# Optimization experiments

Hardware: AMD Instinct MI355X
Metric: run time of the kernel (lower is better)

## Reference

```python
import jax, jax.numpy as jnp
import numpy as np

C = 320        # in_channels == inner_dim (n_heads*d_head = 8*40)
HEADS = 8
DH = 40
CTX = 768
FF_INNER = 1280  # 4*C
G = 32         # GroupNorm groups


def _ln(x, w, b, eps=1e-5):
    m = x.mean(-1, keepdims=True)
    v = ((x - m) ** 2).mean(-1, keepdims=True)
    return (x - m) * jax.lax.rsqrt(v + eps) * w + b


def _attn(q, k, v, heads, scale):
    # faithful to source: split last dim as (d h) -> head index is fastest
    B, Lq, D = q.shape
    Lk = k.shape[1]
    dh = D // heads
    q = q.reshape(B, Lq, dh, heads).transpose(0, 3, 1, 2)  # b h i d
    k = k.reshape(B, Lk, dh, heads).transpose(0, 3, 1, 2)  # b h j d
    v = v.reshape(B, Lk, dh, heads).transpose(0, 3, 1, 2)
    sim = jnp.einsum('bhid,bhjd->bhij', q, k) * scale
    w = jax.nn.softmax(sim, axis=-1)
    o = jnp.einsum('bhij,bhjd->bhid', w, v)
    # merge as (h d): head index is slowest on output (matches source)
    return o.transpose(0, 2, 1, 3).reshape(B, Lq, heads * dh)


def setup_inputs() -> dict:
    key = jax.random.key(0)
    ks = jax.random.split(key, 20)
    n = lambda i, shape: jax.random.normal(ks[i], shape, jnp.float32) * 0.02
    z = lambda d: jnp.zeros((d,), jnp.float32)
    o = lambda d: jnp.ones((d,), jnp.float32)
    return dict(
        x=jax.random.normal(ks[0], (1, C, 64, 64), jnp.float32),
        context=jax.random.normal(ks[1], (1, 77, CTX), jnp.float32),
        gn_w=o(C), gn_b=z(C),
        w_in=n(2, (C, C)), b_in=z(C),
        ln1_w=o(C), ln1_b=z(C),
        wq1=n(3, (C, C)), wk1=n(4, (C, C)), wv1=n(5, (C, C)),
        wo1=n(6, (C, C)), bo1=z(C),
        ln2_w=o(C), ln2_b=z(C),
        wq2=n(7, (C, C)), wk2=n(8, (CTX, C)), wv2=n(9, (CTX, C)),
        wo2=n(10, (C, C)), bo2=z(C),
        ln3_w=o(C), ln3_b=z(C),
        wff1=n(11, (C, 2 * FF_INNER)), bff1=z(2 * FF_INNER),
        wff2=n(12, (FF_INNER, C)), bff2=z(C),
        w_out=n(13, (C, C)), b_out=z(C),
    )


def reference(x, context, gn_w, gn_b, w_in, b_in,
              ln1_w, ln1_b, wq1, wk1, wv1, wo1, bo1,
              ln2_w, ln2_b, wq2, wk2, wv2, wo2, bo2,
              ln3_w, ln3_b, wff1, bff1, wff2, bff2,
              w_out, b_out):
    B, Cc, H, W = x.shape
    scale = DH ** (-0.5)
    x_in = x
    # GroupNorm(32, eps=1e-6)
    g = x.reshape(B, G, Cc // G, H, W)
    m = g.mean((2, 3, 4), keepdims=True)
    v = ((g - m) ** 2).mean((2, 3, 4), keepdims=True)
    h = ((g - m) * jax.lax.rsqrt(v + 1e-6)).reshape(B, Cc, H, W)
    h = h * gn_w[None, :, None, None] + gn_b[None, :, None, None]
    # 1x1 conv in_proj
    h = jnp.einsum('bchw,co->bohw', h, w_in) + b_in[None, :, None, None]
    # b c h w -> b (h w) c
    t = h.transpose(0, 2, 3, 1).reshape(B, H * W, C)
    # --- transformer block (depth=1) ---
    # attn_1: self-attn; NOTE source applies k/v proj to the QUERY projection
    hn = _ln(t, ln1_w, ln1_b)
    q = hn @ wq1
    k = q @ wk1
    vv = q @ wv1
    t = t + (_attn(q, k, vv, HEADS, scale) @ wo1 + bo1)
    # attn_2: cross-attn with context
    hn = _ln(t, ln2_w, ln2_b)
    q = hn @ wq2
    k = context @ wk2
    vv = context @ wv2
    t = t + (_attn(q, k, vv, HEADS, scale) @ wo2 + bo2)
    # GEGLU feed-forward
    hn = _ln(t, ln3_w, ln3_b)
    p = hn @ wff1 + bff1
    a, gate = p[..., :FF_INNER], p[..., FF_INNER:]
    t = t + ((a * jax.nn.gelu(gate, approximate=False)) @ wff2 + bff2)
    # b (h w) c -> b c h w
    s = t.reshape(B, H, W, C).transpose(0, 3, 1, 2)
    out = jnp.einsum('bchw,co->bohw', s, w_out) + b_out[None, :, None, None]
    return out + x_in
```

## Files before the change

### kernel.cpp

```cpp
#include <hip/hip_runtime.h>
#include <hip/hip_bf16.h>
#include <math.h>

#define CCH 320
#define NHEADS 8
#define DH 40
#define HW 4096
#define FFI 1280

typedef __bf16 bf16x8 __attribute__((ext_vector_type(8)));
typedef unsigned short u16x8 __attribute__((ext_vector_type(8)));
typedef short s16x4 __attribute__((ext_vector_type(4)));
typedef float f32x4 __attribute__((ext_vector_type(4)));
typedef unsigned int u32x4 __attribute__((ext_vector_type(4)));

#define WQ1BF_OFF 2539520
#define W2_OFF    2641920
#define WT_TOTAL  2949120

__device__ inline unsigned short f2bf(float f) {
    __hip_bfloat16 h = __float2bfloat16(f);
    return __builtin_bit_cast(unsigned short, h);
}
__device__ inline unsigned pk2bf(float a, float b) {
#if __has_builtin(__builtin_amdgcn_cvt_pk_bf16_f32)
    typedef __bf16 bf16x2 __attribute__((ext_vector_type(2)));
    bf16x2 r = __builtin_amdgcn_cvt_pk_bf16_f32(a, b);
    return __builtin_bit_cast(unsigned, r);
#else
    return (unsigned)f2bf(a) | ((unsigned)f2bf(b) << 16);
#endif
}
__device__ inline float bf2f(unsigned short u) {
    return __builtin_bit_cast(float, ((unsigned)u) << 16);
}
__device__ inline bf16x8 ldfrag(const unsigned short* p) {
    u16x8 raw = *reinterpret_cast<const u16x8*>(p);
    return __builtin_bit_cast(bf16x8, raw);
}
__device__ inline s16x4 pk2frag(unsigned a, unsigned b) {
    unsigned long long v = (unsigned long long)a | ((unsigned long long)b << 32);
    return __builtin_bit_cast(s16x4, v);
}

__device__ inline float ex2(float x) {
#if __has_builtin(__builtin_amdgcn_exp2f)
    return __builtin_amdgcn_exp2f(x);
#else
    return exp2f(x);
#endif
}
__device__ inline float fast_rcp(float x) {
#if __has_builtin(__builtin_amdgcn_rcpf)
    return __builtin_amdgcn_rcpf(x);
#else
    return 1.f / x;
#endif
}
__device__ inline float fast_gelu(float x) {
    float z = fabsf(x) * 0.70710678118654752f;
    float t = fast_rcp(fmaf(0.3275911f, z, 1.f));
    float poly = fmaf(fmaf(fmaf(fmaf(1.061405429f, t, -1.453152027f), t,
                               1.421413741f), t, -0.284496736f), t,
                      0.254829592f) * t;
    float e = ex2(z * z * -1.4426950408889634f);
    float erfz = 1.f - poly * e;
    float s = copysignf(erfz, x);
    return 0.5f * x * (1.f + s);
}

__global__ __launch_bounds__(256) void megaprep(
    const float* __restrict__ w_in, const float* __restrict__ wq1,
    const float* __restrict__ wk1, const float* __restrict__ wv1,
    const float* __restrict__ wo1, const float* __restrict__ wq2,
    const float* __restrict__ wo2, const float* __restrict__ w_out,
    const float* __restrict__ wff1, const float* __restrict__ wff2,
    const float* __restrict__ wk2, const float* __restrict__ wv2,
    unsigned short* __restrict__ Wt,
    const float* __restrict__ ctx, unsigned short* __restrict__ ctx_bf,
    const float* __restrict__ X, float2* __restrict__ gnp) {
    __shared__ float tile[64][65];
    __shared__ float s1[256], s2[256];
    const int b = blockIdx.x, tid = threadIdx.x;
    if (b >= 670) {
        if (b < 1054) {
            int idx = (b - 670) * 256 + tid;
            int row = idx / 768, col = idx - row * 768;
            float v = (row < 77) ? ctx[row * 768 + col] : 0.f;
            ctx_bf[idx] = f2bf(v);
        } else {
            const int bg = b - 1054;
            const float* xg = X + bg * 5120;
            float s = 0.f, sq = 0.f;
#pragma unroll
            for (int i = 0; i < 20; ++i) { float v = xg[tid + i * 256]; s += v; sq += v * v; }
            s1[tid] = s; s2[tid] = sq; __syncthreads();
            for (int off = 128; off > 0; off >>= 1) {
                if (tid < off) { s1[tid] += s1[tid + off]; s2[tid] += s2[tid + off]; }
                __syncthreads();
            }
            if (tid == 0) gnp[bg] = make_float2(s1[0], s2[0]);
        }
        return;
    }
    if (b >= 620 && b < 645) {
        int t = b - 620;
        int base = (t / 5) * 64 * 320 + (t % 5) * 64;
#pragma unroll
        for (int i = 0; i < 16; ++i) {
            int idx = tid + i * 256;
            int r = idx >> 6, cn = idx & 63;
            Wt[WQ1BF_OFF + base + r * 320 + cn] = f2bf(wq1[base + r * 320 + cn]);
        }
        return;
    }
    const float* src;
    int K, stride, dstoff, k0, n0;
    bool glu = false;
    if (b < 200) {
        int m = b / 25, t = b % 25;
        k0 = (t / 5) * 64; n0 = (t % 5) * 64;
        K = 320; stride = 320; dstoff = m * 102400;
        src = (m == 0) ? w_in : (m == 1) ? wq1 : (m == 2) ? wk1 :
              (m == 3) ? wv1 : (m == 4) ? wo1 : (m == 5) ? wq2 :
              (m == 6) ? wo2 : w_out;
    } else if (b < 300) {
        int t = b - 200;
        k0 = (t / 5) * 64; n0 = (t % 5) * 64;
        K = 1280; stride = 320; dstoff = 1638400; src = wff2;
    } else if (b < 500) {
        int t = b - 300;
        k0 = (t / 40) * 64; n0 = (t % 40) * 64;
        K = 320; stride = 2560; dstoff = 819200; src = wff1; glu = true;
    } else if (b < 560) {
        int t = b - 500;
        k0 = (t / 5) * 64; n0 = (t % 5) * 64;
        K = 768; stride = 320; dstoff = 2048000; src = wk2;
    } else if (b < 620) {
        int t = b - 560;
        k0 = (t / 5) * 64; n0 = (t % 5) * 64;
        K = 768; stride = 320; dstoff = 2048000 + 245760; src = wv2;
    } else {
        int t = b - 645;
        k0 = (t / 5) * 64; n0 = (t % 5) * 64;
        K = 320; stride = 320; dstoff = W2_OFF; src = wq1;
    }
#pragma unroll
    for (int i = 0; i < 16; ++i) {
        int idx = tid + i * 256;
        int r = idx >> 6, cn = idx & 63;
        int scol = glu ? ((n0 >> 1) + (cn >> 1) + (cn & 1) * FFI) : (n0 + cn);
        tile[r][cn] = src[(size_t)(k0 + r) * stride + scol];
    }
    __syncthreads();
#pragma unroll
    for (int i = 0; i < 16; ++i) {
        int idx = tid + i * 256;
        int cl = idx >> 6, cr = idx & 63;
        Wt[dstoff + (size_t)(n0 + cl) * K + k0 + cr] = f2bf(tile[cr][cl]);
    }
}

__global__ __launch_bounds__(256) void gn_apply(const float* __restrict__ X,
                                                const float2* __restrict__ part,
                                                const float* __restrict__ w,
                                                const float* __restrict__ b,
                                                unsigned short* __restrict__ Y) {
    __shared__ float tile[64][65];
    __shared__ float gm[32], gr[32];
    const int tid = threadIdx.x;
    const int hw0 = blockIdx.x * 64, c0 = blockIdx.y * 64;
    if (tid < 32) {
        float s = 0.f, sq = 0.f;
#pragma unroll
        for (int i = 0; i < 8; ++i) { float2 p = part[tid * 8 + i]; s += p.x; sq += p.y; }
        float mean = s * (1.f / 40960.f);
        float var  = sq * (1.f / 40960.f) - mean * mean;
        gm[tid] = mean; gr[tid] = rsqrtf(var + 1e-6f);
    }
#pragma unroll
    for (int i = 0; i < 16; ++i) {
        int idx = tid + i * 256;
        int r = idx >> 6, col = idx & 63;
        tile[r][col] = X[(size_t)(c0 + r) * HW + hw0 + col];
    }
    __syncthreads();
#pragma unroll
    for (int i = 0; i < 16; ++i) {
        int idx = tid + i * 256;
        int hwl = idx >> 6, cl = idx & 63;
        int c = c0 + cl, g = c / 10;
        float v = (tile[cl][hwl] - gm[g]) * gr[g] * w[c] + b[c];
        Y[(size_t)(hw0 + hwl) * CCH + c] = f2bf(v);
    }
}

__global__ __launch_bounds__(256) void ln_kernel(const float* __restrict__ X,
                                                 const float* __restrict__ w,
                                                 const float* __restrict__ b,
                                                 unsigned short* __restrict__ Y) {
    const int row  = blockIdx.x * 4 + (threadIdx.x >> 6);
    const int lane = threadIdx.x & 63;
    const float* xr = X + row * CCH;
    const float4 a = *(const float4*)(xr + lane * 4);
    const float  e = xr[256 + lane];
    float v[5] = {a.x, a.y, a.z, a.w, e};
    float s = 0.f, sq = 0.f;
#pragma unroll
    for (int i = 0; i < 5; ++i) { s += v[i]; sq += v[i] * v[i]; }
#pragma unroll
    for (int off = 32; off > 0; off >>= 1) {
        s  += __shfl_xor(s, off, 64);
        sq += __shfl_xor(sq, off, 64);
    }
    const float mean = s * (1.f / 320.f);
    const float var  = sq * (1.f / 320.f) - mean * mean;
    const float rstd = rsqrtf(var + 1e-5f);
    unsigned short* yr = Y + row * CCH;
    const float4 w4 = *(const float4*)(w + lane * 4);
    const float4 b4 = *(const float4*)(b + lane * 4);
    float r0 = (v[0] - mean) * rstd * w4.x + b4.x;
    float r1 = (v[1] - mean) * rstd * w4.y + b4.y;
    float r2 = (v[2] - mean) * rstd * w4.z + b4.z;
    float r3 = (v[3] - mean) * rstd * w4.w + b4.w;
    *(uint2*)(yr + lane * 4) = make_uint2(pk2bf(r0, r1), pk2bf(r2, r3));
    int ct = 256 + lane;
    yr[ct] = f2bf((v[4] - mean) * rstd * w[ct] + b[ct]);
}

template <int MT, int K>
__global__ __launch_bounds__(256) void gemm4(
    const unsigned short* __restrict__ A,
    const unsigned short* __restrict__ Bt,
    const float* __restrict__ bias,
    const float* __restrict__ res,
    void* __restrict__ Cout, void* __restrict__ Cout2,
    int N, int mode, float scale) {
    constexpr int NCH = K / 64;
    __shared__ __align__(16) unsigned short Ab[2][MT * 16 * 64];
    __shared__ __align__(16) unsigned short Bb[2][64 * 64];
    const int tid  = threadIdx.x;
    const int wave = tid >> 6, lane = tid & 63;
    const int quad = lane >> 4, c = lane & 15;
    const int m0 = blockIdx.y * (MT * 16);
    const int bn = blockIdx.x;

    f32x4 acc[MT];
#pragma unroll
    for (int i = 0; i < MT; ++i) acc[i] = (f32x4){0.f, 0.f, 0.f, 0.f};

    const unsigned short* aslab = A + (size_t)m0 * K;
    const unsigned short* bslab = Bt + (size_t)(bn * 64) * K;

    constexpr int ITA = MT * 16 * 8 / 256;
    int arow[ITA], aoff[ITA];
#pragma unroll
    for (int i = 0; i < ITA; ++i) {
        int idx = tid + i * 256;
        arow[i] = idx >> 3;
        int g = idx & 7;
        aoff[i] = arow[i] * 64 + ((g ^ (arow[i] & 7)) * 8);
    }
    int brow[2], boff[2];
#pragma unroll
    for (int i = 0; i < 2; ++i) {
        int idx = tid + i * 256;
        brow[i] = idx >> 3;
        int g = idx & 7;
        boff[i] = brow[i] * 64 + ((g ^ (brow[i] & 7)) * 8);
    }
    const int ag = (tid & 7) * 8;

    {
        u16x8 ra[ITA], rb[2];
#pragma unroll
        for (int i = 0; i < ITA; ++i)
            ra[i] = *(const u16x8*)(aslab + (size_t)arow[i] * K + ag);
#pragma unroll
        for (int i = 0; i < 2; ++i)
            rb[i] = *(const u16x8*)(bslab + (size_t)brow[i] * K + ag);
#pragma unroll
        for (int i = 0; i < ITA; ++i) *(u16x8*)&Ab[0][aoff[i]] = ra[i];
#pragma unroll
        for (int i = 0; i < 2; ++i) *(u16x8*)&Bb[0][boff[i]] = rb[i];
    }
    __syncthreads();

    const int swz0 = (quad ^ (c & 7)) * 8;
    const int swz1 = ((quad + 4) ^ (c & 7)) * 8;
#pragma unroll
    for (int ch = 0; ch < NCH; ++ch) {
        const int buf = ch & 1;
        u16x8 ra[ITA], rb[2];
        if (ch + 1 < NCH) {
            const int kb = (ch + 1) * 64;
#pragma unroll
            for (int i = 0; i < ITA; ++i)
                ra[i] = *(const u16x8*)(aslab + (size_t)arow[i] * K + kb + ag);
#pragma unroll
            for (int i = 0; i < 2; ++i)
                rb[i] = *(const u16x8*)(bslab + (size_t)brow[i] * K + kb + ag);
        }
        bf16x8 b0 = ldfrag(&Bb[buf][(wave * 16 + c) * 64 + swz0]);
        bf16x8 b1 = ldfrag(&Bb[buf][(wave * 16 + c) * 64 + swz1]);
#pragma unroll
        for (int mt = 0; mt < MT; ++mt) {
            bf16x8 a0 = ldfrag(&Ab[buf][(mt * 16 + c) * 64 + swz0]);
            bf16x8 a1 = ldfrag(&Ab[buf][(mt * 16 + c) * 64 + swz1]);
            acc[mt] = __builtin_amdgcn_mfma_f32_16x16x32_bf16(a0, b0, acc[mt], 0, 0, 0);
            acc[mt] = __builtin_amdgcn_mfma_f32_16x16x32_bf16(a1, b1, acc[mt], 0, 0, 0);
        }
        if (ch + 1 < NCH) {
            const int nb = buf ^ 1;
#pragma unroll
            for (int i = 0; i < ITA; ++i) *(u16x8*)&Ab[nb][aoff[i]] = ra[i];
#pragma unroll
            for (int i = 0; i < 2; ++i) *(u16x8*)&Bb[nb][boff[i]] = rb[i];
        }
        __syncthreads();
    }

    const int col = bn * 64 + wave * 16 + c;
    float bval = 0.f;
    if (bias) bval = (mode == 5) ? bias[(col >> 1) + (col & 1) * FFI] : bias[col];

    if (mode == 9) {
#pragma unroll
        for (int mt = 0; mt < MT; ++mt) {
            const int row0 = m0 + mt * 16 + quad * 4;
            float4 xv = *(const float4*)(res + (size_t)col * HW + row0);
            float4 ov;
            ov.x = acc[mt][0] + bval + xv.x;
            ov.y = acc[mt][1] + bval + xv.y;
            ov.z = acc[mt][2] + bval + xv.z;
            ov.w = acc[mt][3] + bval + xv.w;
            *(float4*)((float*)Cout + (size_t)col * HW + row0) = ov;
        }
        return;
    }
#pragma unroll
    for (int mt = 0; mt < MT; ++mt) {
#pragma unroll
        for (int r = 0; r < 4; ++r) {
            const int row = m0 + mt * 16 + quad * 4 + r;
            float v = acc[mt][r];
            if (mode == 0) {
                v += bval;
                if (res) v += res[(size_t)row * N + col];
                ((float*)Cout)[(size_t)row * N + col] = v;
            } else if (mode == 2) {
                int h = col & 7, d = col >> 3;
                ((unsigned short*)Cout)[(((size_t)h << 12) + row) * 64 + d] = f2bf(v * scale);
                if (d < 24)
                    ((unsigned short*)Cout)[(((size_t)h << 12) + row) * 64 + 40 + d] = 0;
            } else if (mode == 4) {
                ((unsigned short*)Cout)[(size_t)row * N + col] =
                    f2bf(v + bval + res[(size_t)row * N + col]);
            } else if (mode == 5) {
                v += bval;
                float other = __shfl_xor(v, 1, 64);
                if ((c & 1) == 0) {
                    float g = fast_gelu(other);
                    ((unsigned short*)Cout)[(size_t)row * FFI + (col >> 1)] = f2bf(v * g);
                }
            } else if (mode == 8) {
                if (col < 320) {
                    int h = col & 7, d = col >> 3;
                    ((unsigned short*)Cout)[(((size_t)h << 7) + row) * 64 + d] = f2bf(v);
                    if (d < 24)
                        ((unsigned short*)Cout)[(((size_t)h << 7) + row) * 64 + 40 + d] = 0;
                } else {
                    int c2 = col - 320;
                    int h = c2 & 7, d = c2 >> 3;
                    ((unsigned short*)Cout2)[(size_t)(h * 48 + d) * 128 + row] = f2bf(v);
                    if (d < 8)
                        ((unsigned short*)Cout2)[(size_t)(h * 48 + 40 + d) * 128 + row] =
                            (d == 0) ? (unsigned short)0x3F80 : (unsigned short)0;
                }
            } else if (mode == 10) {
                ((unsigned short*)Cout)[(size_t)col * 320 + row] = f2bf(v);
            } else {
                if (col < 320) {
                    int h = col & 7, d = col >> 3;
                    ((unsigned short*)Cout)[(((size_t)h << 12) + row) * 64 + d] = f2bf(v * scale);
                    if (d < 24)
                        ((unsigned short*)Cout)[(((size_t)h << 12) + row) * 64 + 40 + d] = 0;
                } else if (col < 640) {
                    int c2 = col - 320;
                    int h = c2 & 7, d = c2 >> 3;
                    ((unsigned short*)Cout2)[(((size_t)h << 12) + row) * 64 + d] = f2bf(v);
                    if (d < 24)
                        ((unsigned short*)Cout2)[(((size_t)h << 12) + row) * 64 + 40 + d] = 0;
                } else {
                    int c2 = col - 640;
                    int h = c2 & 7, d = c2 >> 3;
                    unsigned short* Vt_ = (unsigned short*)Cout2 + (size_t)8 * 4096 * 64;
                    Vt_[(((size_t)(h * 48 + d)) << 12) + row] = f2bf(v);
                    if (d < 8)
                        Vt_[(((size_t)(h * 48 + 40 + d)) << 12) + row] =
                            (d == 0) ? (unsigned short)0x3F80 : (unsigned short)0;
                }
            }
        }
    }
}

template <int TILES, bool MASK, bool FINAL>
__global__ __launch_bounds__(256) void attn8(
    const unsigned short* __restrict__ Qp,
    const unsigned short* __restrict__ Kp,
    const unsigned short* __restrict__ Vt,
    float* __restrict__ pO, float* __restrict__ pL,
    unsigned short* __restrict__ Ofin,
    int Lk, int Lkp) {
    __shared__ __align__(16) unsigned short Kb[2][64 * 64];
    __shared__ __align__(16) unsigned short Vb[2][48 * 64];
    const int tid  = threadIdx.x;
    const int wave = tid >> 6, lane = tid & 63;
    const int quad = lane >> 4, c = lane & 15;
    const int id  = blockIdx.x;
    const int h   = id & 7;
    const int qt  = (id >> 3) & 31;
    const int seg = id >> 8;
    const int q0  = qt * 128 + wave * 32;

    const unsigned short* qbaseA = Qp + ((((size_t)h << 12) + q0 + c) << 6) + quad * 8;
    const bf16x8 bQA0 = ldfrag(qbaseA);
    const bf16x8 bQA1 = ldfrag(qbaseA + 32);
    const bf16x8 bQB0 = ldfrag(qbaseA + 1024);
    const bf16x8 bQB1 = ldfrag(qbaseA + 1024 + 32);

    f32x4 oA[3], oB[3];
#pragma unroll
    for (int i = 0; i < 3; ++i) {
        oA[i] = (f32x4){0.f, 0.f, 0.f, 0.f};
        oB[i] = (f32x4){0.f, 0.f, 0.f, 0.f};
    }

    const int kt0 = seg * TILES;
    const unsigned short* kglob = Kp + (((size_t)h * Lkp + kt0 * 64) << 6);
    const unsigned short* vglob = Vt + ((size_t)h * 48) * Lkp + kt0 * 64;

    const int r0 = lane >> 3;
    const int g  = lane & 7;
    int ldsoff[4];
    const unsigned short* gptr0[4];
#pragma unroll
    for (int i = 0; i < 4; ++i) {
        int s = wave + 4 * i;
        if (s < 8) {
            int row = s * 8 + r0;
            ldsoff[i] = row * 64 + (g ^ (row & 7)) * 8;
            gptr0[i]  = kglob + (size_t)row * 64 + g * 8;
        } else if (s < 14) {
            int d = (s - 8) * 8 + r0;
            ldsoff[i] = d * 64 + (g ^ (d & 7)) * 8;
            gptr0[i]  = vglob + (size_t)d * Lkp + g * 8;
        } else {
            ldsoff[i] = 0; gptr0[i] = nullptr;
        }
    }
    const bool isK[4] = {(wave + 0) < 8, (wave + 4) < 8, (wave + 8) < 8, (wave + 12) < 8};
    const bool act[4] = {true, true, true, (wave + 12) < 14};

    {
        u16x8 st[4];
#pragma unroll
        for (int i = 0; i < 4; ++i)
            if (act[i]) st[i] = *(const u16x8*)(gptr0[i]);
#pragma unroll
        for (int i = 0; i < 4; ++i)
            if (act[i]) {
                unsigned short* lp = isK[i] ? &Kb[0][ldsoff[i]] : &Vb[0][ldsoff[i]];
                *(u16x8*)lp = st[i];
            }
    }
    __syncthreads();

#pragma unroll
    for (int t = 0; t < TILES; ++t) {
        const int b = t & 1;
        u16x8 st[4];
        if (t + 1 < TILES) {
            const int kb = (t + 1) * 64;
#pragma unroll
            for (int i = 0; i < 4; ++i)
                if (act[i]) {
                    const unsigned short* gp =
                        isK[i] ? (gptr0[i] + (size_t)kb * 64) : (gptr0[i] + kb);
                    st[i] = *(const u16x8*)gp;
                }
        }
        const unsigned short* Kl = &Kb[b][0];
        const unsigned short* Vl = &Vb[b][0];
        const int sw0 = (quad ^ (c & 7)) * 8;
        const int sw1 = ((quad + 4) ^ (c & 7)) * 8;
        const int abs_kb = kt0 * 64 + t * 64;
#pragma unroll
        for (int blk = 0; blk < 4; ++blk) {
            const int row = (blk * 16 + c) * 64;
            bf16x8 k0 = ldfrag(Kl + row + sw0);
            bf16x8 k1 = ldfrag(Kl + row + sw1);
            f32x4 zA = {0.f, 0.f, 0.f, 0.f};
            zA = __builtin_amdgcn_mfma_f32_16x16x32_bf16(k0, bQA0, zA, 0, 0, 0);
            zA = __builtin_amdgcn_mfma_f32_16x16x32_bf16(k1, bQA1, zA, 0, 0, 0);
            f32x4 zB = {0.f, 0.f, 0.f, 0.f};
            zB = __builtin_amdgcn_mfma_f32_16x16x32_bf16(k0, bQB0, zB, 0, 0, 0);
            zB = __builtin_amdgcn_mfma_f32_16x16x32_bf16(k1, bQB1, zB, 0, 0, 0);
            if (MASK) {
#pragma unroll
                for (int r = 0; r < 4; ++r) {
                    bool inv = (abs_kb + blk * 16 + quad * 4 + r >= Lk);
                    zA[r] = inv ? -30000.f : zA[r];
                    zB[r] = inv ? -30000.f : zB[r];
                }
            }
            s16x4 PA = pk2frag(pk2bf(ex2(zA[0]), ex2(zA[1])),
                               pk2bf(ex2(zA[2]), ex2(zA[3])));
            s16x4 PB = pk2frag(pk2bf(ex2(zB[0]), ex2(zB[1])),
                               pk2bf(ex2(zB[2]), ex2(zB[3])));
#pragma unroll
            for (int db = 0; db < 3; ++db) {
                const int dim = db * 16 + c;
                const int off =
                    (((blk * 2 + (quad >> 1)) ^ (dim & 7)) * 8) + (quad & 1) * 4;
                s16x4 vf = *(const s16x4*)(Vl + dim * 64 + off);
                oA[db] = __builtin_amdgcn_mfma_f32_16x16x16bf16_1k(vf, PA, oA[db], 0, 0, 0);
                oB[db] = __builtin_amdgcn_mfma_f32_16x16x16bf16_1k(vf, PB, oB[db], 0, 0, 0);
            }
        }
        if (t + 1 < TILES) {
            const int nb = b ^ 1;
#pragma unroll
            for (int i = 0; i < 4; ++i)
                if (act[i]) {
                    unsigned short* lp = isK[i] ? &Kb[nb][ldsoff[i]] : &Vb[nb][ldsoff[i]];
                    *(u16x8*)lp = st[i];
                }
        }
        __syncthreads();
    }
    if (FINAL) {
        float lA = __shfl(oA[2][0], 32 + c, 64);
        float lB = __shfl(oB[2][0], 32 + c, 64);
        float liA = fast_rcp(lA), liB = fast_rcp(lB);
        unsigned short* oaptr = Ofin + (size_t)(q0 + c) * CCH + h * DH;
        unsigned short* obptr = Ofin + (size_t)(q0 + 16 + c) * CCH + h * DH;
        *(uint2*)(oaptr + quad * 4) =
            make_uint2(pk2bf(oA[0][0] * liA, oA[0][1] * liA),
                       pk2bf(oA[0][2] * liA, oA[0][3] * liA));
        *(uint2*)(oaptr + 16 + quad * 4) =
            make_uint2(pk2bf(oA[1][0] * liA, oA[1][1] * liA),
                       pk2bf(oA[1][2] * liA, oA[1][3] * liA));
        if (quad < 2)
            *(uint2*)(oaptr + 32 + quad * 4) =
                make_uint2(pk2bf(oA[2][0] * liA, oA[2][1] * liA),
                           pk2bf(oA[2][2] * liA, oA[2][3] * liA));
        *(uint2*)(obptr + quad * 4) =
            make_uint2(pk2bf(oB[0][0] * liB, oB[0][1] * liB),
                       pk2bf(oB[0][2] * liB, oB[0][3] * liB));
        *(uint2*)(obptr + 16 + quad * 4) =
            make_uint2(pk2bf(oB[1][0] * liB, oB[1][1] * liB),
                       pk2bf(oB[1][2] * liB, oB[1][3] * liB));
        if (quad < 2)
            *(uint2*)(obptr + 32 + quad * 4) =
                make_uint2(pk2bf(oB[2][0] * liB, oB[2][1] * liB),
                           pk2bf(oB[2][2] * liB, oB[2][3] * liB));
        return;
    }
    const size_t base = ((size_t)(seg * 8 + h)) << 12;
    float* obA = pO + (base + q0 + c) * 40;
    *(float4*)(obA + quad * 4)      = make_float4(oA[0][0], oA[0][1], oA[0][2], oA[0][3]);
    *(float4*)(obA + 16 + quad * 4) = make_float4(oA[1][0], oA[1][1], oA[1][2], oA[1][3]);
    if (quad < 2)
        *(float4*)(obA + 32 + quad * 4) = make_float4(oA[2][0], oA[2][1], oA[2][2], oA[2][3]);
    float* obB = pO + (base + q0 + 16 + c) * 40;
    *(float4*)(obB + quad * 4)      = make_float4(oB[0][0], oB[0][1], oB[0][2], oB[0][3]);
    *(float4*)(obB + 16 + quad * 4) = make_float4(oB[1][0], oB[1][1], oB[1][2], oB[1][3]);
    if (quad < 2)
        *(float4*)(obB + 32 + quad * 4) = make_float4(oB[2][0], oB[2][1], oB[2][2], oB[2][3]);
    if (quad == 2) {
        pL[base + q0 + c]      = oA[2][0];
        pL[base + q0 + 16 + c] = oB[2][0];
    }
}

__global__ __launch_bounds__(256) void attn_combine2(
    const float* __restrict__ pO, const float* __restrict__ pL,
    unsigned short* __restrict__ O, int S) {
    int idx = blockIdx.x * 256 + threadIdx.x;
    int h = idx / (HW * 10);
    int rem = idx - h * (HW * 10);
    int row = rem / 10, dg = rem - row * 10;
    float4 num = make_float4(0.f, 0.f, 0.f, 0.f);
    float den = 0.f;
    for (int s = 0; s < S; ++s) {
        size_t base = ((size_t)(s * 8 + h)) << 12;
        float4 p = *(const float4*)(pO + (base + row) * 40 + dg * 4);
        num.x += p.x; num.y += p.y; num.z += p.z; num.w += p.w;
        den += pL[base + row];
    }
    float inv = fast_rcp(den);
    unsigned short* ob = O + (size_t)row * CCH + h * DH + dg * 4;
    unsigned lo = pk2bf(num.x * inv, num.y * inv);
    unsigned hi = pk2bf(num.z * inv, num.w * inv);
    *(uint2*)ob = make_uint2(lo, hi);
}

extern "C" void kernel_launch(void* const* d_in, const int* in_sizes, int n_in,
                              void* d_out, int out_size, void* d_ws, size_t ws_size,
                              hipStream_t stream) {
    const float* x     = (const float*)d_in[0];
    const float* ctx   = (const float*)d_in[1];
    const float* gn_w  = (const float*)d_in[2];
    const float* gn_b  = (const float*)d_in[3];
    const float* w_in  = (const float*)d_in[4];
    const float* b_in  = (const float*)d_in[5];
    const float* ln1_w = (const float*)d_in[6];
    const float* ln1_b = (const float*)d_in[7];
    const float* wq1   = (const float*)d_in[8];
    const float* wk1   = (const float*)d_in[9];
    const float* wv1   = (const float*)d_in[10];
    const float* wo1   = (const float*)d_in[11];
    const float* bo1   = (const float*)d_in[12];
    const float* ln2_w = (const float*)d_in[13];
    const float* ln2_b = (const float*)d_in[14];
    const float* wq2   = (const float*)d_in[15];
    const float* wk2   = (const float*)d_in[16];
    const float* wv2   = (const float*)d_in[17];
    const float* wo2   = (const float*)d_in[18];
    const float* bo2   = (const float*)d_in[19];
    const float* ln3_w = (const float*)d_in[20];
    const float* ln3_b = (const float*)d_in[21];
    const float* wff1  = (const float*)d_in[22];
    const float* bff1  = (const float*)d_in[23];
    const float* wff2  = (const float*)d_in[24];
    const float* bff2  = (const float*)d_in[25];
    const float* w_out = (const float*)d_in[26];
    const float* b_out = (const float*)d_in[27];
    float* out = (float*)d_out;

    const int NT = HW * CCH;
    const size_t u16_cnt = (size_t)NT * 3 + (size_t)HW * FFI +
                           (size_t)8 * 4096 * 64 * 2 + (size_t)8 * 48 * 4096 +
                           8 * 128 * 64 + 8 * 48 * 128 + WT_TOTAL + 128 * 768;
    const size_t need8 = (size_t)4 * (NT + 8 * NT + 8 * 32768 + 512) +
                         2 * u16_cnt + 4096;
    const int SEGS = (ws_size >= need8) ? 8 : 4;

    float* ws = (float*)d_ws;
    float* t_   = ws;
    float* pO   = t_ + NT;
    float* pL   = pO + (size_t)SEGS * NT;
    float2* gnp = (float2*)(pL + (size_t)SEGS * 8 * 4096);
    unsigned short* u = (unsigned short*)(gnp + 256);
    unsigned short* a_bf = u;                  u += NT;
    unsigned short* o_bf = u;                  u += NT;
    unsigned short* t_bf = u;                  u += NT;
    unsigned short* g_bf = u;                  u += HW * FFI;
    unsigned short* Qp   = u;                  u += 8 * 4096 * 64;
    unsigned short* Kp   = u;                  u += 8 * 4096 * 64;
    unsigned short* Vt   = u;                  u += 8 * 48 * 4096;
    unsigned short* Kc   = u;                  u += 8 * 128 * 64;
    unsigned short* Vc   = u;                  u += 8 * 48 * 128;
    unsigned short* Wt   = u;                  u += WT_TOTAL;
    unsigned short* ctx_bf = u;                u += 128 * 768;

    const unsigned short* w_inT  = Wt;
    const unsigned short* wo1T   = Wt + 409600;
    const unsigned short* wq2T   = Wt + 512000;
    const unsigned short* wo2T   = Wt + 614400;
    const unsigned short* w_outT = Wt + 716800;
    const unsigned short* wff1T  = Wt + 819200;
    const unsigned short* wff2T  = Wt + 1638400;
    const unsigned short* wk2T   = Wt + 2048000;
    const unsigned short* wk1T   = Wt + 204800;
    const unsigned short* Wq1bf  = Wt + WQ1BF_OFF;
    unsigned short*       W2     = Wt + W2_OFF;

    const float qscale = 0.15811388300841897f * 1.4426950408889634f;

    megaprep<<<1310, 256, 0, stream>>>(w_in, wq1, wk1, wv1, wo1, wq2, wo2, w_out,
                                       wff1, wff2, wk2, wv2, Wt, ctx, ctx_bf,
                                       x, gnp);
    gemm4<2, 320><<<dim3(10, 10), 256, 0, stream>>>(
        Wq1bf, wk1T, nullptr, nullptr, W2 + (size_t)320 * 320, nullptr, 640, 10, 1.f);
    gn_apply<<<dim3(64, 5), 256, 0, stream>>>(x, gnp, gn_w, gn_b, a_bf);
    gemm4<2, 320><<<dim3(5, 128), 256, 0, stream>>>(a_bf, w_inT, b_in, nullptr, t_, nullptr, CCH, 0, 1.f);
    ln_kernel<<<1024, 256, 0, stream>>>(t_, ln1_w, ln1_b, a_bf);
    gemm4<2, 320><<<dim3(15, 128), 256, 0, stream>>>(a_bf, W2, nullptr, nullptr, Qp, Kp, 960, 11, qscale);
    if (SEGS == 8)
        attn8<8, false, false><<<2048, 256, 0, stream>>>(Qp, Kp, Vt, pO, pL, nullptr, HW, HW);
    else
        attn8<16, false, false><<<1024, 256, 0, stream>>>(Qp, Kp, Vt, pO, pL, nullptr, HW, HW);
    attn_combine2<<<1280, 256, 0, stream>>>(pO, pL, o_bf, SEGS);
    gemm4<2, 320><<<dim3(5, 128), 256, 0, stream>>>(o_bf, wo1T, bo1, t_, t_, nullptr, CCH, 0, 1.f);
    ln_kernel<<<1024, 256, 0, stream>>>(t_, ln2_w, ln2_b, a_bf);
    gemm4<2, 320><<<dim3(5, 128), 256, 0, stream>>>(a_bf, wq2T, nullptr, nullptr, Qp, nullptr, CCH, 2, qscale);
    gemm4<2, 768><<<dim3(10, 4), 256, 0, stream>>>(ctx_bf, wk2T, nullptr, nullptr, Kc, Vc, 640, 8, 1.f);
    attn8<2, true, true><<<256, 256, 0, stream>>>(Qp, Kc, Vc, nullptr, nullptr, o_bf, 77, 128);
    gemm4<2, 320><<<dim3(5, 128), 256, 0, stream>>>(o_bf, wo2T, bo2, t_, t_, nullptr, CCH, 0, 1.f);
    ln_kernel<<<1024, 256, 0, stream>>>(t_, ln3_w, ln3_b, a_bf);
    gemm4<2, 320><<<dim3(40, 128), 256, 0, stream>>>(a_bf, wff1T, bff1, nullptr, g_bf, nullptr, 2 * FFI, 5, 1.f);
    gemm4<2, 1280><<<dim3(5, 128), 256, 0, stream>>>(g_bf, wff2T, bff2, t_, t_bf, nullptr, CCH, 4, 1.f);
    gemm4<2, 320><<<dim3(5, 128), 256, 0, stream>>>(t_bf, w_outT, b_out, x, out, nullptr, CCH, 9, 1.f);
}
```

Before: 294.2 us.

## Fuse LayerNorm into GEMMs via atomic row statistics from producer epilogues

```diff
diff --git a/kernel.cpp b/kernel.cpp
--- a/kernel.cpp
+++ b/kernel.cpp
@@ -69,6 +69,23 @@
     return 0.5f * x * (1.f + s);
 }
 
+__device__ inline u16x8 ln_pack(const float* ar, float mean, float rs,
+                                const float* wp, const float* bp) {
+    float4 x0 = *(const float4*)ar, x1 = *(const float4*)(ar + 4);
+    float4 w0 = *(const float4*)wp, w1 = *(const float4*)(wp + 4);
+    float4 b0 = *(const float4*)bp, b1 = *(const float4*)(bp + 4);
+    unsigned r0 = pk2bf((x0.x - mean) * rs * w0.x + b0.x,
+                        (x0.y - mean) * rs * w0.y + b0.y);
+    unsigned r1 = pk2bf((x0.z - mean) * rs * w0.z + b0.z,
+                        (x0.w - mean) * rs * w0.w + b0.w);
+    unsigned r2 = pk2bf((x1.x - mean) * rs * w1.x + b1.x,
+                        (x1.y - mean) * rs * w1.y + b1.y);
+    unsigned r3 = pk2bf((x1.z - mean) * rs * w1.z + b1.z,
+                        (x1.w - mean) * rs * w1.w + b1.w);
+    u32x4 u = {r0, r1, r2, r3};
+    return __builtin_bit_cast(u16x8, u);
+}
+
 __global__ __launch_bounds__(256) void megaprep(
     const float* __restrict__ w_in, const float* __restrict__ wq1,
     const float* __restrict__ wk1, const float* __restrict__ wv1,
@@ -78,10 +95,16 @@
     const float* __restrict__ wk2, const float* __restrict__ wv2,
     unsigned short* __restrict__ Wt,
     const float* __restrict__ ctx, unsigned short* __restrict__ ctx_bf,
-    const float* __restrict__ X, float2* __restrict__ gnp) {
+    const float* __restrict__ X, float2* __restrict__ gnp,
+    float* __restrict__ lnst) {
     __shared__ float tile[64][65];
     __shared__ float s1[256], s2[256];
     const int b = blockIdx.x, tid = threadIdx.x;
+    if (b >= 1310) {
+        int idx = (b - 1310) * 256 + tid;
+        *(float4*)(lnst + (size_t)idx * 4) = make_float4(0.f, 0.f, 0.f, 0.f);
+        return;
+    }
     if (b >= 670) {
         if (b < 1054) {
             int idx = (b - 670) * 256 + tid;
@@ -195,42 +218,14 @@
     }
 }
 
-__global__ __launch_bounds__(256) void ln_kernel(const float* __restrict__ X,
-                                                 const float* __restrict__ w,
-                                                 const float* __restrict__ b,
-                                                 unsigned short* __restrict__ Y) {
-    const int row  = blockIdx.x * 4 + (threadIdx.x >> 6);
-    const int lane = threadIdx.x & 63;
-    const float* xr = X + row * CCH;
-    const float4 a = *(const float4*)(xr + lane * 4);
-    const float  e = xr[256 + lane];
-    float v[5] = {a.x, a.y, a.z, a.w, e};
-    float s = 0.f, sq = 0.f;
-#pragma unroll
-    for (int i = 0; i < 5; ++i) { s += v[i]; sq += v[i] * v[i]; }
-#pragma unroll
-    for (int off = 32; off > 0; off >>= 1) {
-        s  += __shfl_xor(s, off, 64);
-        sq += __shfl_xor(sq, off, 64);
-    }
-    const float mean = s * (1.f / 320.f);
-    const float var  = sq * (1.f / 320.f) - mean * mean;
-    const float rstd = rsqrtf(var + 1e-5f);
-    unsigned short* yr = Y + row * CCH;
-    const float4 w4 = *(const float4*)(w + lane * 4);
-    const float4 b4 = *(const float4*)(b + lane * 4);
-    float r0 = (v[0] - mean) * rstd * w4.x + b4.x;
-    float r1 = (v[1] - mean) * rstd * w4.y + b4.y;
-    float r2 = (v[2] - mean) * rstd * w4.z + b4.z;
-    float r3 = (v[3] - mean) * rstd * w4.w + b4.w;
-    *(uint2*)(yr + lane * 4) = make_uint2(pk2bf(r0, r1), pk2bf(r2, r3));
-    int ct = 256 + lane;
-    yr[ct] = f2bf((v[4] - mean) * rstd * w[ct] + b[ct]);
-}
-
-template <int MT, int K>
+template <int MT, int K, bool LNA = false>
 __global__ __launch_bounds__(256) void gemm4(
     const unsigned short* __restrict__ A,
+    const float* __restrict__ Af,
+    const float* __restrict__ lnw,
+    const float* __restrict__ lnb,
+    const float* __restrict__ lnstats,
+    float* __restrict__ ostats,
     const unsigned short* __restrict__ Bt,
     const float* __restrict__ bias,
     const float* __restrict__ res,
@@ -249,7 +244,8 @@
 #pragma unroll
     for (int i = 0; i < MT; ++i) acc[i] = (f32x4){0.f, 0.f, 0.f, 0.f};
 
-    const unsigned short* aslab = A + (size_t)m0 * K;
+    const unsigned short* aslab = LNA ? nullptr : A + (size_t)m0 * K;
+    const float* afslab = LNA ? Af + (size_t)m0 * K : nullptr;
     const unsigned short* bslab = Bt + (size_t)(bn * 64) * K;
 
     constexpr int ITA = MT * 16 * 8 / 256;
@@ -271,11 +267,28 @@
     }
     const int ag = (tid & 7) * 8;
 
+    float meanA[ITA], rsA[ITA];
+    if constexpr (LNA) {
+#pragma unroll
+        for (int i = 0; i < ITA; ++i) {
+            float2 st = *(const float2*)(lnstats + (size_t)(m0 + arow[i]) * 2);
+            float mean = st.x * (1.f / 320.f);
+            float var  = st.y * (1.f / 320.f) - mean * mean;
+            meanA[i] = mean;
+            rsA[i]   = rsqrtf(var + 1e-5f);
+        }
+    }
+
     {
         u16x8 ra[ITA], rb[2];
 #pragma unroll
-        for (int i = 0; i < ITA; ++i)
-            ra[i] = *(const u16x8*)(aslab + (size_t)arow[i] * K + ag);
+        for (int i = 0; i < ITA; ++i) {
+            if constexpr (LNA)
+                ra[i] = ln_pack(afslab + (size_t)arow[i] * K + ag, meanA[i], rsA[i],
+                                lnw + ag, lnb + ag);
+            else
+                ra[i] = *(const u16x8*)(aslab + (size_t)arow[i] * K + ag);
+        }
 #pragma unroll
         for (int i = 0; i < 2; ++i)
             rb[i] = *(const u16x8*)(bslab + (size_t)brow[i] * K + ag);
@@ -295,8 +308,13 @@
         if (ch + 1 < NCH) {
             const int kb = (ch + 1) * 64;
 #pragma unroll
-            for (int i = 0; i < ITA; ++i)
-                ra[i] = *(const u16x8*)(aslab + (size_t)arow[i] * K + kb + ag);
+            for (int i = 0; i < ITA; ++i) {
+                if constexpr (LNA)
+                    ra[i] = ln_pack(afslab + (size_t)arow[i] * K + kb + ag,
+                                    meanA[i], rsA[i], lnw + kb + ag, lnb + kb + ag);
+                else
+                    ra[i] = *(const u16x8*)(aslab + (size_t)arow[i] * K + kb + ag);
+            }
 #pragma unroll
             for (int i = 0; i < 2; ++i)
                 rb[i] = *(const u16x8*)(bslab + (size_t)brow[i] * K + kb + ag);
@@ -338,6 +356,7 @@
         }
         return;
     }
+    float vv[MT][4];
 #pragma unroll
     for (int mt = 0; mt < MT; ++mt) {
 #pragma unroll
@@ -348,6 +367,7 @@
                 v += bval;
                 if (res) v += res[(size_t)row * N + col];
                 ((float*)Cout)[(size_t)row * N + col] = v;
+                vv[mt][r] = v;
             } else if (mode == 2) {
                 int h = col & 7, d = col >> 3;
                 ((unsigned short*)Cout)[(((size_t)h << 12) + row) * 64 + d] = f2bf(v * scale);
@@ -403,6 +423,24 @@
             }
         }
     }
+    if (mode == 0 && ostats) {
+#pragma unroll
+        for (int mt = 0; mt < MT; ++mt)
+#pragma unroll
+            for (int r = 0; r < 4; ++r) {
+                float s = vv[mt][r], sq = s * s;
+#pragma unroll
+                for (int off = 1; off <= 8; off <<= 1) {
+                    s  += __shfl_xor(s, off, 64);
+                    sq += __shfl_xor(sq, off, 64);
+                }
+                if (c == 0) {
+                    const int row = m0 + mt * 16 + quad * 4 + r;
+                    atomicAdd(&ostats[(size_t)row * 2], s);
+                    atomicAdd(&ostats[(size_t)row * 2 + 1], sq);
+                }
+            }
+    }
 }
 
 template <int TILES, bool MASK, bool FINAL>
@@ -645,7 +683,7 @@
                            (size_t)8 * 4096 * 64 * 2 + (size_t)8 * 48 * 4096 +
                            8 * 128 * 64 + 8 * 48 * 128 + WT_TOTAL + 128 * 768;
     const size_t need8 = (size_t)4 * (NT + 8 * NT + 8 * 32768 + 512) +
-                         2 * u16_cnt + 4096;
+                         102400 + 2 * u16_cnt + 4096;
     const int SEGS = (ws_size >= need8) ? 8 : 4;
 
     float* ws = (float*)d_ws;
@@ -653,7 +691,8 @@
     float* pO   = t_ + NT;
     float* pL   = pO + (size_t)SEGS * NT;
     float2* gnp = (float2*)(pL + (size_t)SEGS * 8 * 4096);
-    unsigned short* u = (unsigned short*)(gnp + 256);
+    float* lnst = (float*)(gnp + 256);
+    unsigned short* u = (unsigned short*)(lnst + 24576);
     unsigned short* a_bf = u;                  u += NT;
     unsigned short* o_bf = u;                  u += NT;
     unsigned short* t_bf = u;                  u += NT;
@@ -666,6 +705,10 @@
     unsigned short* Wt   = u;                  u += WT_TOTAL;
     unsigned short* ctx_bf = u;                u += 128 * 768;
 
+    float* lnst0 = lnst;
+    float* lnst1 = lnst + 8192;
+    float* lnst2 = lnst + 16384;
+
     const unsigned short* w_inT  = Wt;
     const unsigned short* wo1T   = Wt + 409600;
     const unsigned short* wq2T   = Wt + 512000;
@@ -680,28 +723,44 @@
 
     const float qscale = 0.15811388300841897f * 1.4426950408889634f;
 
-    megaprep<<<1310, 256, 0, stream>>>(w_in, wq1, wk1, wv1, wo1, wq2, wo2, w_out,
+    megaprep<<<1334, 256, 0, stream>>>(w_in, wq1, wk1, wv1, wo1, wq2, wo2, w_out,
                                        wff1, wff2, wk2, wv2, Wt, ctx, ctx_bf,
-                                       x, gnp);
+                                       x, gnp, lnst);
     gemm4<2, 320><<<dim3(10, 10), 256, 0, stream>>>(
-        Wq1bf, wk1T, nullptr, nullptr, W2 + (size_t)320 * 320, nullptr, 640, 10, 1.f);
+        Wq1bf, nullptr, nullptr, nullptr, nullptr, nullptr,
+        wk1T, nullptr, nullptr, W2 + (size_t)320 * 320, nullptr, 640, 10, 1.f);
     gn_apply<<<dim3(64, 5), 256, 0, stream>>>(x, gnp, gn_w, gn_b, a_bf);
-    gemm4<2, 320><<<dim3(5, 128), 256, 0, stream>>>(a_bf, w_inT, b_in, nullptr, t_, nullptr, CCH, 0, 1.f);
-    ln_kernel<<<1024, 256, 0, stream>>>(t_, ln1_w, ln1_b, a_bf);
-    gemm4<2, 320><<<dim3(15, 128), 256, 0, stream>>>(a_bf, W2, nullptr, nullptr, Qp, Kp, 960, 11, qscale);
+    gemm4<2, 320><<<dim3(5, 128), 256, 0, stream>>>(
+        a_bf, nullptr, nullptr, nullptr, nullptr, lnst0,
+        w_inT, b_in, nullptr, t_, nullptr, CCH, 0, 1.f);
+    gemm4<2, 320, true><<<dim3(15, 128), 256, 0, stream>>>(
+        nullptr, t_, ln1_w, ln1_b, lnst0, nullptr,
+        W2, nullptr, nullptr, Qp, Kp, 960, 11, qscale);
     if (SEGS == 8)
         attn8<8, false, false><<<2048, 256, 0, stream>>>(Qp, Kp, Vt, pO, pL, nullptr, HW, HW);
     else
         attn8<16, false, false><<<1024, 256, 0, stream>>>(Qp, Kp, Vt, pO, pL, nullptr, HW, HW);
     attn_combine2<<<1280, 256, 0, stream>>>(pO, pL, o_bf, SEGS);
-    gemm4<2, 320><<<dim3(5, 128), 256, 0, stream>>>(o_bf, wo1T, bo1, t_, t_, nullptr, CCH, 0, 1.f);
-    ln_kernel<<<1024, 256, 0, stream>>>(t_, ln2_w, ln2_b, a_bf);
-    gemm4<2, 320><<<dim3(5, 128), 256, 0, stream>>>(a_bf, wq2T, nullptr, nullptr, Qp, nullptr, CCH, 2, qscale);
-    gemm4<2, 768><<<dim3(10, 4), 256, 0, stream>>>(ctx_bf, wk2T, nullptr, nullptr, Kc, Vc, 640, 8, 1.f);
+    gemm4<2, 320><<<dim3(5, 128), 256, 0, stream>>>(
+        o_bf, nullptr, nullptr, nullptr, nullptr, lnst1,
+        wo1T, bo1, t_, t_, nullptr, CCH, 0, 1.f);
+    gemm4<2, 320, true><<<dim3(5, 128), 256, 0, stream>>>(
+        nullptr, t_, ln2_w, ln2_b, lnst1, nullptr,
+        wq2T, nullptr, nullptr, Qp, nullptr, CCH, 2, qscale);
+    gemm4<2, 768><<<dim3(10, 4), 256, 0, stream>>>(
+        ctx_bf, nullptr, nullptr, nullptr, nullptr, nullptr,
+        wk2T, nullptr, nullptr, Kc, Vc, 640, 8, 1.f);
     attn8<2, true, true><<<256, 256, 0, stream>>>(Qp, Kc, Vc, nullptr, nullptr, o_bf, 77, 128);
-    gemm4<2, 320><<<dim3(5, 128), 256, 0, stream>>>(o_bf, wo2T, bo2, t_, t_, nullptr, CCH, 0, 1.f);
-    ln_kernel<<<1024, 256, 0, stream>>>(t_, ln3_w, ln3_b, a_bf);
-    gemm4<2, 320><<<dim3(40, 128), 256, 0, stream>>>(a_bf, wff1T, bff1, nullptr, g_bf, nullptr, 2 * FFI, 5, 1.f);
-    gemm4<2, 1280><<<dim3(5, 128), 256, 0, stream>>>(g_bf, wff2T, bff2, t_, t_bf, nullptr, CCH, 4, 1.f);
-    gemm4<2, 320><<<dim3(5, 128), 256, 0, stream>>>(t_bf, w_outT, b_out, x, out, nullptr, CCH, 9, 1.f);
-}
+    gemm4<2, 320><<<dim3(5, 128), 256, 0, stream>>>(
+        o_bf, nullptr, nullptr, nullptr, nullptr, lnst2,
+        wo2T, bo2, t_, t_, nullptr, CCH, 0, 1.f);
+    gemm4<2, 320, true><<<dim3(40, 128), 256, 0, stream>>>(
+        nullptr, t_, ln3_w, ln3_b, lnst2, nullptr,
+        wff1T, bff1, nullptr, g_bf, nullptr, 2 * FFI, 5, 1.f);
+    gemm4<2, 1280><<<dim3(5, 128), 256, 0, stream>>>(
+        g_bf, nullptr, nullptr, nullptr, nullptr, nullptr,
+        wff2T, bff2, t_, t_bf, nullptr, CCH, 4, 1.f);
+    gemm4<2, 320><<<dim3(5, 128), 256, 0, stream>>>(
+        t_bf, nullptr, nullptr, nullptr, nullptr, nullptr,
+        w_outT, b_out, x, out, nullptr, CCH, 9, 1.f);
+}
```

After: 321.6 us. 9.3% more time.
